# Optimization experiments

Hardware: AMD Instinct MI355X
Metric: run time of the kernel (lower is better)

## Reference

```python
import jax, jax.numpy as jnp
import numpy as np

E = 8
DIMS = [512, 1024, 1024, 512]
BATCH = 2048


def _init_w(key, shape):
    a = np.sqrt(6.0 / (shape[-2] * shape[-1]))
    return jax.random.uniform(key, shape, dtype=jnp.float32, minval=-a, maxval=a)


def setup_inputs() -> dict:
    key = jax.random.key(0)
    ks = jax.random.split(key, 8)
    inp = {
        "weight_blend": jax.random.uniform(ks[0], (BATCH, E), dtype=jnp.float32),
        "x": jax.random.normal(ks[1], (BATCH, DIMS[0]), dtype=jnp.float32),
    }
    for i in range(3):
        inp[f"W{i}"] = _init_w(ks[2 + i], (E, DIMS[i + 1], DIMS[i]))
        inp[f"B{i}"] = jnp.zeros((E, DIMS[i + 1], 1), dtype=jnp.float32)
    return inp


def reference(weight_blend, x, W0, B0, W1, B1, W2, B2):
    Ws = [W0, W1, W2]
    Bs = [B0, B1, B2]
    acts = [jax.nn.elu, jax.nn.elu, None]
    for W, B, act in zip(Ws, Bs, acts):
        # dropout p=0 -> identity
        # blended-expert GEMM: sum_e wb[b,e] * (W[e] @ x[b]) == einsum
        t = jnp.einsum("be,eoi,bi->bo", weight_blend, W, x)
        bias = jnp.einsum("be,eo->bo", weight_blend, B[..., 0])
        x = t + bias
        if act is not None:
            x = act(x)
    return x
```

## Files before the change

### kernel.cpp

```cpp
#include <hip/hip_runtime.h>
#include <math.h>

typedef __attribute__((ext_vector_type(8))) short bf16x8;
typedef __attribute__((ext_vector_type(4))) float f32x4;

#define NEXP 8
#define BATCH 2048

__device__ __forceinline__ unsigned short f2bf(float f) {
    union { float f; unsigned u; } v; v.f = f;
    unsigned r = v.u + 0x7FFFu + ((v.u >> 16) & 1u);
    return (unsigned short)(r >> 16);
}

__global__ __launch_bounds__(256) void pack_all(
    const float* __restrict__ W0, const float* __restrict__ W1,
    const float* __restrict__ W2, const float* __restrict__ x,
    unsigned short* __restrict__ W0p, unsigned short* __restrict__ W1p,
    unsigned short* __restrict__ W2p, unsigned short* __restrict__ x0p)
{
    __shared__ float T[128 * 36];
    const int bid = blockIdx.x, t = threadIdx.x;

    if (bid < 10240) {
        const float* W; unsigned short* out; int KB, Din, Dout, U, lin;
        if (bid < 2048)      { W = W0; out = W0p; KB = 16; Din = 512;  Dout = 1024; U = 4; lin = bid; }
        else if (bid < 6144) { W = W1; out = W1p; KB = 32; Din = 1024; Dout = 1024; U = 4; lin = bid - 2048; }
        else                 { W = W2; out = W2p; KB = 32; Din = 1024; Dout = 512;  U = 2; lin = bid - 6144; }
        const int e  = lin & 7;
        const int r  = lin >> 3;
        const int kb = r % KB;
        const int nb = r / KB;
        const int N0 = nb * 16 * U;
        const int K0 = kb * 32;
        for (int it = 0; it < U / 2; ++it) {
            const int idx = t + 256 * it;
            const int nl = idx >> 3, k4 = (idx & 7) * 4;
            float4 v = *(const float4*)(W + ((size_t)e * Dout + N0 + nl) * Din + K0 + k4);
            *(float4*)(T + nl * 36 + k4) = v;
        }
        __syncthreads();
        if (t < 64 * U) {
            const int u = t >> 6, l = t & 63;
            const float* p = T + (u * 16 + (l & 15)) * 36 + (l >> 4) * 8;
            bf16x8 h;
            #pragma unroll
            for (int j = 0; j < 8; ++j) h[j] = (short)f2bf(p[j]);
            *(bf16x8*)(out + (size_t)lin * (U * 512) + t * 8) = h;
        }
    } else {
        const int lin = bid - 10240;
        const int kb = lin & 15, mb = lin >> 4;
        for (int it = 0; it < 4; ++it) {
            const int idx = t + 256 * it;
            const int ml = idx >> 3, k4 = (idx & 7) * 4;
            float4 v = *(const float4*)(x + (size_t)(mb * 128 + ml) * 512 + kb * 32 + k4);
            *(float4*)(T + ml * 36 + k4) = v;
        }
        __syncthreads();
        #pragma unroll
        for (int it = 0; it < 2; ++it) {
            const int s = t + 256 * it;
            const int g = s >> 6, l = s & 63;
            const float* p = T + (g * 16 + (l & 15)) * 36 + (l >> 4) * 8;
            bf16x8 h;
            #pragma unroll
            for (int j = 0; j < 8; ++j) h[j] = (short)f2bf(p[j]);
            *(bf16x8*)(x0p + (size_t)lin * 4096 + s * 8) = h;
        }
    }
}

template<int UP>
__global__ __launch_bounds__(256, 3) void moe_mfma6(
    const unsigned short* __restrict__ Xp,
    const unsigned short* __restrict__ Wp,
    const float* __restrict__ Bias,
    const float* __restrict__ WBl,
    void* __restrict__ Yout,
    int KB, int Dout, int KBn, int act, int packed_out)
{
    constexpr int PSTR = 36;
    __shared__ __align__(16) float lds_f[2 * 64 * PSTR];

    const int tid  = threadIdx.x;
    const int ew   = tid >> 6;
    const int l    = tid & 63;
    const int lh   = l >> 4;
    const int ll   = l & 15;
    const int e0   = 2 * ew;
    const int bx   = blockIdx.x;
    const int by   = blockIdx.y;
    const int m0   = by * 64;
    const int n0   = bx * 32;
    const int mb   = by >> 1;
    const int half = by & 1;

    f32x4 acc0[4][2], acc1[4][2];
    #pragma unroll
    for (int t = 0; t < 4; ++t)
        #pragma unroll
        for (int u = 0; u < 2; ++u)
            #pragma unroll
            for (int i = 0; i < 4; ++i) { acc0[t][u][i] = 0.f; acc1[t][u][i] = 0.f; }

    unsigned aoff[4];
    #pragma unroll
    for (int t = 0; t < 4; ++t)
        aoff[t] = (unsigned)(mb * KB) * 8192u + (unsigned)(half * 4 + t) * 1024u + l * 16u;
    const int nb   = (bx * 2) / UP;
    const int uoff = (bx * 2) % UP;
    unsigned boff0[2], boff1[2];
    #pragma unroll
    for (int u = 0; u < 2; ++u) {
        boff0[u] = (((unsigned)(nb * KB) * 8 + e0) * UP + uoff + u) * 1024u + l * 16u;
        boff1[u] = boff0[u] + UP * 1024u;
    }
    const unsigned astr = 8192u;
    const unsigned bstr = UP * 8192u;
    const char* xc = (const char*)Xp;
    const char* wc = (const char*)Wp;

    bf16x8 aR[2][4], b0R[2][2], b1R[2][2];

    auto LOAD = [&](int s, int kk) {
        const unsigned ab = (unsigned)kk * astr;
        const unsigned bb = (unsigned)kk * bstr;
        #pragma unroll
        for (int t = 0; t < 4; ++t)
            aR[s][t] = *(const bf16x8*)(xc + aoff[t] + ab);
        #pragma unroll
        for (int u = 0; u < 2; ++u) {
            b0R[s][u] = *(const bf16x8*)(wc + boff0[u] + bb);
            b1R[s][u] = *(const bf16x8*)(wc + boff1[u] + bb);
        }
    };
    auto MF = [&](int s) {
        #pragma unroll
        for (int u = 0; u < 2; ++u)
            #pragma unroll
            for (int t = 0; t < 4; ++t) {
                acc0[t][u] = __builtin_amdgcn_mfma_f32_16x16x32_bf16(aR[s][t], b0R[s][u], acc0[t][u], 0, 0, 0);
                acc1[t][u] = __builtin_amdgcn_mfma_f32_16x16x32_bf16(aR[s][t], b1R[s][u], acc1[t][u], 0, 0, 0);
            }
    };

    LOAD(0, 0);
    for (int kk = 0; kk < KB; kk += 2) {
        if (kk + 1 < KB) LOAD(1, kk + 1);
        MF(0);
        if (kk + 2 < KB) LOAD(0, kk + 2);
        MF(1);
    }

    float bi0[2], bi1[2];
    #pragma unroll
    for (int u = 0; u < 2; ++u) {
        const int n = n0 + u * 16 + ll;
        bi0[u] = Bias[(size_t)e0 * Dout + n];
        bi1[u] = Bias[(size_t)(e0 + 1) * Dout + n];
    }

    float* pb = lds_f + (ew & 1) * (64 * PSTR);

    if (ew < 2) {
        #pragma unroll
        for (int t = 0; t < 4; ++t)
            #pragma unroll
            for (int r = 0; r < 4; ++r) {
                const int lm = 16 * t + 4 * lh + r;
                float2 wbp = ((const float2*)(WBl + (size_t)(m0 + lm) * NEXP))[ew];
                #pragma unroll
                for (int u = 0; u < 2; ++u)
                    pb[lm * PSTR + u * 16 + ll] =
                        wbp.x * (acc0[t][u][r] + bi0[u]) + wbp.y * (acc1[t][u][r] + bi1[u]);
            }
    }
    __syncthreads();
    if (ew >= 2) {
        #pragma unroll
        for (int t = 0; t < 4; ++t)
            #pragma unroll
            for (int r = 0; r < 4; ++r) {
                const int lm = 16 * t + 4 * lh + r;
                float2 wbp = ((const float2*)(WBl + (size_t)(m0 + lm) * NEXP))[ew];
                #pragma unroll
                for (int u = 0; u < 2; ++u)
                    pb[lm * PSTR + u * 16 + ll] +=
                        wbp.x * (acc0[t][u][r] + bi0[u]) + wbp.y * (acc1[t][u][r] + bi1[u]);
            }
    }
    __syncthreads();

    float* pb0 = lds_f;
    float* pb1 = lds_f + 64 * PSTR;
    if (packed_out) {
        const int g  = tid >> 6;
        const int c0 = lh * 8;
        const int rowbase = (g * 16 + ll) * PSTR;
        bf16x8 h;
        #pragma unroll
        for (int j = 0; j < 8; ++j) {
            float v = pb0[rowbase + c0 + j] + pb1[rowbase + c0 + j];
            if (act) v = v > 0.f ? v : expm1f(v);
            h[j] = (short)f2bf(v);
        }
        unsigned short* dst = (unsigned short*)Yout +
            ((size_t)(mb * KBn + bx) * 8 + half * 4 + g) * 512 + l * 8;
        *(bf16x8*)dst = h;
    } else {
        #pragma unroll
        for (int it = 0; it < 2; ++it) {
            const int idx = tid + 256 * it;
            const int row = idx >> 3;
            const int c4  = (idx & 7) * 4;
            float4 s = *(const float4*)(pb0 + row * PSTR + c4);
            float4 q = *(const float4*)(pb1 + row * PSTR + c4);
            s.x += q.x; s.y += q.y; s.z += q.z; s.w += q.w;
            if (act) {
                s.x = s.x > 0.f ? s.x : expm1f(s.x);
                s.y = s.y > 0.f ? s.y : expm1f(s.y);
                s.z = s.z > 0.f ? s.z : expm1f(s.z);
                s.w = s.w > 0.f ? s.w : expm1f(s.w);
            }
            *(float4*)((float*)Yout + (size_t)(m0 + row) * Dout + n0 + c4) = s;
        }
    }
}

#define BM 64
#define BNF 64
#define BKF 16
#define PAD 4

__global__ __launch_bounds__(256) void moe_layer_f32(
    const float* __restrict__ X, const float* __restrict__ W,
    const float* __restrict__ Bias, const float* __restrict__ WB,
    float* __restrict__ Y, int Din, int Dout, int act)
{
    __shared__ float As[BKF][BM + PAD];
    __shared__ float Bs[BKF][BNF + PAD];
    const int tid = threadIdx.x;
    const int tm = tid >> 4, tn = tid & 15;
    const int m0 = blockIdx.y * BM, n0 = blockIdx.x * BNF;
    const int lr = tid >> 2, lc = (tid & 3) << 2;
    float acc[4][4] = {};
    const float* xrow  = X  + (size_t)(m0 + lr) * Din;
    const float* wbrow = WB + (size_t)(m0 + lr) * NEXP;
    const float* wrow0 = W  + (size_t)(n0 + lr) * Din;
    for (int e = 0; e < NEXP; ++e) {
        const float wbe = wbrow[e];
        const float* wrow = wrow0 + (size_t)e * Dout * Din;
        for (int k0 = 0; k0 < Din; k0 += BKF) {
            float4 av = *(const float4*)(xrow + k0 + lc);
            float4 bv = *(const float4*)(wrow + k0 + lc);
            __syncthreads();
            As[lc+0][lr] = av.x*wbe; As[lc+1][lr] = av.y*wbe;
            As[lc+2][lr] = av.z*wbe; As[lc+3][lr] = av.w*wbe;
            Bs[lc+0][lr] = bv.x; Bs[lc+1][lr] = bv.y;
            Bs[lc+2][lr] = bv.z; Bs[lc+3][lr] = bv.w;
            __syncthreads();
            #pragma unroll
            for (int k = 0; k < BKF; ++k) {
                float4 a = *(const float4*)&As[k][tm << 2];
                float4 b = *(const float4*)&Bs[k][tn << 2];
                acc[0][0]+=a.x*b.x; acc[0][1]+=a.x*b.y; acc[0][2]+=a.x*b.z; acc[0][3]+=a.x*b.w;
                acc[1][0]+=a.y*b.x; acc[1][1]+=a.y*b.y; acc[1][2]+=a.y*b.z; acc[1][3]+=a.y*b.w;
                acc[2][0]+=a.z*b.x; acc[2][1]+=a.z*b.y; acc[2][2]+=a.z*b.z; acc[2][3]+=a.z*b.w;
                acc[3][0]+=a.w*b.x; acc[3][1]+=a.w*b.y; acc[3][2]+=a.w*b.z; acc[3][3]+=a.w*b.w;
            }
        }
    }
    #pragma unroll
    for (int im = 0; im < 4; ++im) {
        const int m = m0 + (tm << 2) + im;
        const float* wbm = WB + (size_t)m * NEXP;
        float wv[NEXP];
        #pragma unroll
        for (int e = 0; e < NEXP; ++e) wv[e] = wbm[e];
        #pragma unroll
        for (int in = 0; in < 4; ++in) {
            const int n = n0 + (tn << 2) + in;
            float bsum = 0.f;
            #pragma unroll
            for (int e = 0; e < NEXP; ++e) bsum += wv[e] * Bias[(size_t)e * Dout + n];
            float v = acc[im][in] + bsum;
            if (act) v = v > 0.f ? v : expm1f(v);
            acc[im][in] = v;
        }
        float4 o = make_float4(acc[im][0], acc[im][1], acc[im][2], acc[im][3]);
        *(float4*)(Y + (size_t)m * Dout + n0 + (tn << 2)) = o;
    }
}

extern "C" void kernel_launch(void* const* d_in, const int* in_sizes, int n_in,
                              void* d_out, int out_size, void* d_ws, size_t ws_size,
                              hipStream_t stream)
{
    (void)in_sizes; (void)n_in; (void)out_size;
    const float* wb = (const float*)d_in[0];
    const float* x  = (const float*)d_in[1];
    const float* W0 = (const float*)d_in[2];
    const float* B0 = (const float*)d_in[3];
    const float* W1 = (const float*)d_in[4];
    const float* B1 = (const float*)d_in[5];
    const float* W2 = (const float*)d_in[6];
    const float* B2 = (const float*)d_in[7];
    float* out = (float*)d_out;

    const size_t NW0 = (size_t)8*1024*512, NW1 = (size_t)8*1024*1024, NW2 = (size_t)8*512*1024;
    const size_t NX0 = (size_t)BATCH*512, NX1 = (size_t)BATCH*1024;
    const size_t need = (NW0 + NW1 + NW2 + NX0 + 2 * NX1) * 2;

    if (ws_size >= need) {
        unsigned short* W0p = (unsigned short*)d_ws;
        unsigned short* W1p = W0p + NW0;
        unsigned short* W2p = W1p + NW1;
        unsigned short* x0p = W2p + NW2;
        unsigned short* x1p = x0p + NX0;
        unsigned short* x2p = x1p + NX1;
        pack_all<<<10496, 256, 0, stream>>>(W0, W1, W2, x, W0p, W1p, W2p, x0p);
        moe_mfma6<4><<<dim3(32, 32), 256, 0, stream>>>(x0p, W0p, B0, wb, x1p, 16, 1024, 32, 1, 1);
        moe_mfma6<4><<<dim3(32, 32), 256, 0, stream>>>(x1p, W1p, B1, wb, x2p, 32, 1024, 32, 1, 1);
        moe_mfma6<2><<<dim3(16, 32), 256, 0, stream>>>(x2p, W2p, B2, wb, out, 32, 512,  0, 0, 0);
    } else {
        float* x1 = (float*)d_ws;
        float* x2 = x1 + (size_t)BATCH * 1024;
        moe_layer_f32<<<dim3(1024/BNF, BATCH/BM), 256, 0, stream>>>(x,  W0, B0, wb, x1, 512,  1024, 1);
        moe_layer_f32<<<dim3(1024/BNF, BATCH/BM), 256, 0, stream>>>(x1, W1, B1, wb, x2, 1024, 1024, 1);
        moe_layer_f32<<<dim3(512/BNF,  BATCH/BM), 256, 0, stream>>>(x2, W2, B2, wb, out, 1024, 512,  0);
    }
}
```

Before: 201.8 us.

## Switch MoE GEMMs to 32x32x16 MFMA with new packing and split-K last layer

```diff
diff --git a/kernel.cpp b/kernel.cpp
--- a/kernel.cpp
+++ b/kernel.cpp
@@ -1,8 +1,8 @@
 #include <hip/hip_runtime.h>
 #include <math.h>
 
-typedef __attribute__((ext_vector_type(8))) short bf16x8;
-typedef __attribute__((ext_vector_type(4))) float f32x4;
+typedef __attribute__((ext_vector_type(8)))  short bf16x8;
+typedef __attribute__((ext_vector_type(16))) float f32x16;
 
 #define NEXP 8
 #define BATCH 2048
@@ -13,136 +13,124 @@
     return (unsigned short)(r >> 16);
 }
 
-__global__ __launch_bounds__(256) void pack_all(
+__global__ __launch_bounds__(256) void pack32(
     const float* __restrict__ W0, const float* __restrict__ W1,
     const float* __restrict__ W2, const float* __restrict__ x,
     unsigned short* __restrict__ W0p, unsigned short* __restrict__ W1p,
     unsigned short* __restrict__ W2p, unsigned short* __restrict__ x0p)
 {
-    __shared__ float T[128 * 36];
-    const int bid = blockIdx.x, t = threadIdx.x;
-
-    if (bid < 10240) {
-        const float* W; unsigned short* out; int KB, Din, Dout, U, lin;
-        if (bid < 2048)      { W = W0; out = W0p; KB = 16; Din = 512;  Dout = 1024; U = 4; lin = bid; }
-        else if (bid < 6144) { W = W1; out = W1p; KB = 32; Din = 1024; Dout = 1024; U = 4; lin = bid - 2048; }
-        else                 { W = W2; out = W2p; KB = 32; Din = 1024; Dout = 512;  U = 2; lin = bid - 6144; }
-        const int e  = lin & 7;
-        const int r  = lin >> 3;
-        const int kb = r % KB;
-        const int nb = r / KB;
-        const int N0 = nb * 16 * U;
-        const int K0 = kb * 32;
-        for (int it = 0; it < U / 2; ++it) {
-            const int idx = t + 256 * it;
-            const int nl = idx >> 3, k4 = (idx & 7) * 4;
-            float4 v = *(const float4*)(W + ((size_t)e * Dout + N0 + nl) * Din + K0 + k4);
-            *(float4*)(T + nl * 36 + k4) = v;
-        }
-        __syncthreads();
-        if (t < 64 * U) {
-            const int u = t >> 6, l = t & 63;
-            const float* p = T + (u * 16 + (l & 15)) * 36 + (l >> 4) * 8;
-            bf16x8 h;
-            #pragma unroll
-            for (int j = 0; j < 8; ++j) h[j] = (short)f2bf(p[j]);
-            *(bf16x8*)(out + (size_t)lin * (U * 512) + t * 8) = h;
-        }
+    __shared__ float T[32 * 260];
+    const int bid = blockIdx.x, tid = threadIdx.x;
+
+    const float* src; unsigned short* out;
+    int Din, rowbase, kc, KBw, lin_nb_e_base; bool isx = false;
+    if (bid < 512) {
+        int c = bid;            const int e = c & 7, kcl = (c >> 3) & 1, nb = c >> 4;
+        src = W0; out = W0p; Din = 512; KBw = 32; kc = kcl;
+        rowbase = e * 1024 + nb * 32; lin_nb_e_base = (nb * KBw) * 8 + e;
+    } else if (bid < 1536) {
+        int c = bid - 512;      const int e = c & 7, kcl = (c >> 3) & 3, nb = c >> 5;
+        src = W1; out = W1p; Din = 1024; KBw = 64; kc = kcl;
+        rowbase = e * 1024 + nb * 32; lin_nb_e_base = (nb * KBw) * 8 + e;
+    } else if (bid < 2048) {
+        int c = bid - 1536;     const int e = c & 7, kcl = (c >> 3) & 3, nb = c >> 5;
+        src = W2; out = W2p; Din = 1024; KBw = 64; kc = kcl;
+        rowbase = e * 512 + nb * 32; lin_nb_e_base = (nb * KBw) * 8 + e;
     } else {
-        const int lin = bid - 10240;
-        const int kb = lin & 15, mb = lin >> 4;
-        for (int it = 0; it < 4; ++it) {
-            const int idx = t + 256 * it;
-            const int ml = idx >> 3, k4 = (idx & 7) * 4;
-            float4 v = *(const float4*)(x + (size_t)(mb * 128 + ml) * 512 + kb * 32 + k4);
-            *(float4*)(T + ml * 36 + k4) = v;
-        }
-        __syncthreads();
-        #pragma unroll
-        for (int it = 0; it < 2; ++it) {
-            const int s = t + 256 * it;
-            const int g = s >> 6, l = s & 63;
-            const float* p = T + (g * 16 + (l & 15)) * 36 + (l >> 4) * 8;
-            bf16x8 h;
-            #pragma unroll
-            for (int j = 0; j < 8; ++j) h[j] = (short)f2bf(p[j]);
-            *(bf16x8*)(x0p + (size_t)lin * 4096 + s * 8) = h;
-        }
-    }
-}
-
-template<int UP>
-__global__ __launch_bounds__(256, 3) void moe_mfma6(
+        int c = bid - 2048;     const int kcl = c & 1, mb = c >> 1;
+        src = x; out = x0p; Din = 512; KBw = 32; kc = kcl;
+        rowbase = mb * 32; lin_nb_e_base = mb * 32; isx = true;
+    }
+
+    #pragma unroll
+    for (int it = 0; it < 8; ++it) {
+        const int idx = tid + 256 * it;
+        const int row = idx >> 6, c4 = idx & 63;
+        float4 v = *(const float4*)(src + (size_t)(rowbase + row) * Din + kc * 256 + c4 * 4);
+        *(float4*)(T + row * 260 + c4 * 4) = v;
+    }
+    __syncthreads();
+    #pragma unroll
+    for (int it = 0; it < 4; ++it) {
+        const int s = tid + 256 * it;
+        const int f = s >> 6, l = s & 63;
+        const float* p = T + (l & 31) * 260 + f * 16 + (l >> 5) * 8;
+        bf16x8 h;
+        #pragma unroll
+        for (int j = 0; j < 8; ++j) h[j] = (short)f2bf(p[j]);
+        const int lin = isx ? (lin_nb_e_base + kc * 16 + f)
+                            : (lin_nb_e_base + (kc * 16 + f) * 8);
+        *(bf16x8*)(out + (size_t)lin * 512 + l * 8) = h;
+    }
+}
+
+__global__ __launch_bounds__(256, 2) void moe_gemm32(
     const unsigned short* __restrict__ Xp,
     const unsigned short* __restrict__ Wp,
     const float* __restrict__ Bias,
     const float* __restrict__ WBl,
     void* __restrict__ Yout,
-    int KB, int Dout, int KBn, int act, int packed_out)
-{
-    constexpr int PSTR = 36;
-    __shared__ __align__(16) float lds_f[2 * 64 * PSTR];
-
-    const int tid  = threadIdx.x;
-    const int ew   = tid >> 6;
-    const int l    = tid & 63;
-    const int lh   = l >> 4;
-    const int ll   = l & 15;
-    const int e0   = 2 * ew;
-    const int bx   = blockIdx.x;
-    const int by   = blockIdx.y;
-    const int m0   = by * 64;
-    const int n0   = bx * 32;
-    const int mb   = by >> 1;
-    const int half = by & 1;
-
-    f32x4 acc0[4][2], acc1[4][2];
-    #pragma unroll
-    for (int t = 0; t < 4; ++t)
-        #pragma unroll
-        for (int u = 0; u < 2; ++u)
-            #pragma unroll
-            for (int i = 0; i < 4; ++i) { acc0[t][u][i] = 0.f; acc1[t][u][i] = 0.f; }
-
-    unsigned aoff[4];
-    #pragma unroll
-    for (int t = 0; t < 4; ++t)
-        aoff[t] = (unsigned)(mb * KB) * 8192u + (unsigned)(half * 4 + t) * 1024u + l * 16u;
-    const int nb   = (bx * 2) / UP;
-    const int uoff = (bx * 2) % UP;
-    unsigned boff0[2], boff1[2];
-    #pragma unroll
-    for (int u = 0; u < 2; ++u) {
-        boff0[u] = (((unsigned)(nb * KB) * 8 + e0) * UP + uoff + u) * 1024u + l * 16u;
-        boff1[u] = boff0[u] + UP * 1024u;
-    }
-    const unsigned astr = 8192u;
-    const unsigned bstr = UP * 8192u;
+    int KB, int kk0, int Dout, int KBx, int KBn, int act,
+    int addbias, int packed_out)
+{
+    __shared__ __align__(16) float lds_f[2 * 64 * 68];
+
+    const int tid = threadIdx.x;
+    const int ew  = tid >> 6;
+    const int l   = tid & 63;
+    const int ln  = l & 31;
+    const int lk  = l >> 5;
+    const int e0  = 2 * ew;
+    const int bx  = blockIdx.x;
+    const int by  = blockIdx.y;
+    const int m0  = by * 64;
+    const int n0  = bx * 64;
+
+    f32x16 acc[2][2][2];
+    #pragma unroll
+    for (int e = 0; e < 2; ++e)
+        #pragma unroll
+        for (int t = 0; t < 2; ++t)
+            #pragma unroll
+            for (int u = 0; u < 2; ++u)
+                #pragma unroll
+                for (int i = 0; i < 16; ++i) acc[e][t][u][i] = 0.f;
+
+    unsigned aoff[2], boff[2][2];
+    #pragma unroll
+    for (int t = 0; t < 2; ++t)
+        aoff[t] = ((unsigned)(by * 2 + t) * KBx + kk0) * 1024u + l * 16u;
+    #pragma unroll
+    for (int u = 0; u < 2; ++u)
+        #pragma unroll
+        for (int e = 0; e < 2; ++e)
+            boff[e][u] = (((unsigned)(bx * 2 + u) * KBx + kk0) * 8 + e0 + e) * 1024u + l * 16u;
     const char* xc = (const char*)Xp;
     const char* wc = (const char*)Wp;
 
-    bf16x8 aR[2][4], b0R[2][2], b1R[2][2];
+    bf16x8 aR[2][2], bR[2][2][2];
 
     auto LOAD = [&](int s, int kk) {
-        const unsigned ab = (unsigned)kk * astr;
-        const unsigned bb = (unsigned)kk * bstr;
-        #pragma unroll
-        for (int t = 0; t < 4; ++t)
+        const unsigned ab = (unsigned)kk * 1024u;
+        const unsigned bb = (unsigned)kk * 8192u;
+        #pragma unroll
+        for (int t = 0; t < 2; ++t)
             aR[s][t] = *(const bf16x8*)(xc + aoff[t] + ab);
         #pragma unroll
-        for (int u = 0; u < 2; ++u) {
-            b0R[s][u] = *(const bf16x8*)(wc + boff0[u] + bb);
-            b1R[s][u] = *(const bf16x8*)(wc + boff1[u] + bb);
-        }
+        for (int e = 0; e < 2; ++e)
+            #pragma unroll
+            for (int u = 0; u < 2; ++u)
+                bR[s][e][u] = *(const bf16x8*)(wc + boff[e][u] + bb);
     };
     auto MF = [&](int s) {
         #pragma unroll
-        for (int u = 0; u < 2; ++u)
-            #pragma unroll
-            for (int t = 0; t < 4; ++t) {
-                acc0[t][u] = __builtin_amdgcn_mfma_f32_16x16x32_bf16(aR[s][t], b0R[s][u], acc0[t][u], 0, 0, 0);
-                acc1[t][u] = __builtin_amdgcn_mfma_f32_16x16x32_bf16(aR[s][t], b1R[s][u], acc1[t][u], 0, 0, 0);
-            }
+        for (int e = 0; e < 2; ++e)
+            #pragma unroll
+            for (int u = 0; u < 2; ++u)
+                #pragma unroll
+                for (int t = 0; t < 2; ++t)
+                    acc[e][t][u] = __builtin_amdgcn_mfma_f32_32x32x16_bf16(
+                        aR[s][t], bR[s][e][u], acc[e][t][u], 0, 0, 0);
     };
 
     LOAD(0, 0);
@@ -153,79 +141,92 @@
         MF(1);
     }
 
-    float bi0[2], bi1[2];
-    #pragma unroll
-    for (int u = 0; u < 2; ++u) {
-        const int n = n0 + u * 16 + ll;
-        bi0[u] = Bias[(size_t)e0 * Dout + n];
-        bi1[u] = Bias[(size_t)(e0 + 1) * Dout + n];
-    }
-
-    float* pb = lds_f + (ew & 1) * (64 * PSTR);
+    float bi[2][2];
+    #pragma unroll
+    for (int e = 0; e < 2; ++e)
+        #pragma unroll
+        for (int u = 0; u < 2; ++u)
+            bi[e][u] = addbias ? Bias[(size_t)(e0 + e) * Dout + n0 + u * 32 + ln] : 0.f;
+
+    float* pb = lds_f + (ew & 1) * (64 * 68);
 
     if (ew < 2) {
         #pragma unroll
-        for (int t = 0; t < 4; ++t)
-            #pragma unroll
-            for (int r = 0; r < 4; ++r) {
-                const int lm = 16 * t + 4 * lh + r;
-                float2 wbp = ((const float2*)(WBl + (size_t)(m0 + lm) * NEXP))[ew];
+        for (int t = 0; t < 2; ++t)
+            #pragma unroll
+            for (int r = 0; r < 16; ++r) {
+                const int row = t * 32 + (r & 3) + 8 * (r >> 2) + 4 * lk;
+                float2 wbp = ((const float2*)(WBl + (size_t)(m0 + row) * NEXP))[ew];
                 #pragma unroll
                 for (int u = 0; u < 2; ++u)
-                    pb[lm * PSTR + u * 16 + ll] =
-                        wbp.x * (acc0[t][u][r] + bi0[u]) + wbp.y * (acc1[t][u][r] + bi1[u]);
+                    pb[row * 68 + u * 32 + ln] =
+                        wbp.x * (acc[0][t][u][r] + bi[0][u]) + wbp.y * (acc[1][t][u][r] + bi[1][u]);
             }
     }
     __syncthreads();
     if (ew >= 2) {
         #pragma unroll
-        for (int t = 0; t < 4; ++t)
-            #pragma unroll
-            for (int r = 0; r < 4; ++r) {
-                const int lm = 16 * t + 4 * lh + r;
-                float2 wbp = ((const float2*)(WBl + (size_t)(m0 + lm) * NEXP))[ew];
+        for (int t = 0; t < 2; ++t)
+            #pragma unroll
+            for (int r = 0; r < 16; ++r) {
+                const int row = t * 32 + (r & 3) + 8 * (r >> 2) + 4 * lk;
+                float2 wbp = ((const float2*)(WBl + (size_t)(m0 + row) * NEXP))[ew];
                 #pragma unroll
                 for (int u = 0; u < 2; ++u)
-                    pb[lm * PSTR + u * 16 + ll] +=
-                        wbp.x * (acc0[t][u][r] + bi0[u]) + wbp.y * (acc1[t][u][r] + bi1[u]);
+                    pb[row * 68 + u * 32 + ln] +=
+                        wbp.x * (acc[0][t][u][r] + bi[0][u]) + wbp.y * (acc[1][t][u][r] + bi[1][u]);
             }
     }
     __syncthreads();
 
     float* pb0 = lds_f;
-    float* pb1 = lds_f + 64 * PSTR;
+    float* pb1 = lds_f + 64 * 68;
     if (packed_out) {
-        const int g  = tid >> 6;
-        const int c0 = lh * 8;
-        const int rowbase = (g * 16 + ll) * PSTR;
-        bf16x8 h;
-        #pragma unroll
-        for (int j = 0; j < 8; ++j) {
-            float v = pb0[rowbase + c0 + j] + pb1[rowbase + c0 + j];
-            if (act) v = v > 0.f ? v : expm1f(v);
-            h[j] = (short)f2bf(v);
-        }
-        unsigned short* dst = (unsigned short*)Yout +
-            ((size_t)(mb * KBn + bx) * 8 + half * 4 + g) * 512 + l * 8;
-        *(bf16x8*)dst = h;
+        #pragma unroll
+        for (int it = 0; it < 2; ++it) {
+            const int s = tid + 256 * it;
+            const int f = s >> 6, l2 = s & 63;
+            const int row = (f & 1) * 32 + (l2 & 31);
+            const int cb  = (f >> 1) * 16 + (l2 >> 5) * 8;
+            bf16x8 h;
+            #pragma unroll
+            for (int j = 0; j < 8; ++j) {
+                float v = pb0[row * 68 + cb + j] + pb1[row * 68 + cb + j];
+                if (act) v = v > 0.f ? v : expm1f(v);
+                h[j] = (short)f2bf(v);
+            }
+            const unsigned lin = (unsigned)(by * 2 + (f & 1)) * KBn + bx * 4 + (f >> 1);
+            *(bf16x8*)((unsigned short*)Yout + (size_t)lin * 512 + l2 * 8) = h;
+        }
     } else {
         #pragma unroll
-        for (int it = 0; it < 2; ++it) {
-            const int idx = tid + 256 * it;
-            const int row = idx >> 3;
-            const int c4  = (idx & 7) * 4;
-            float4 s = *(const float4*)(pb0 + row * PSTR + c4);
-            float4 q = *(const float4*)(pb1 + row * PSTR + c4);
-            s.x += q.x; s.y += q.y; s.z += q.z; s.w += q.w;
+        for (int it = 0; it < 4; ++it) {
+            const int s = tid + 256 * it;
+            const int row = s >> 4, c4 = (s & 15) * 4;
+            float4 a = *(const float4*)(pb0 + row * 68 + c4);
+            float4 b = *(const float4*)(pb1 + row * 68 + c4);
+            a.x += b.x; a.y += b.y; a.z += b.z; a.w += b.w;
             if (act) {
-                s.x = s.x > 0.f ? s.x : expm1f(s.x);
-                s.y = s.y > 0.f ? s.y : expm1f(s.y);
-                s.z = s.z > 0.f ? s.z : expm1f(s.z);
-                s.w = s.w > 0.f ? s.w : expm1f(s.w);
-            }
-            *(float4*)((float*)Yout + (size_t)(m0 + row) * Dout + n0 + c4) = s;
-        }
-    }
+                a.x = a.x > 0.f ? a.x : expm1f(a.x);
+                a.y = a.y > 0.f ? a.y : expm1f(a.y);
+                a.z = a.z > 0.f ? a.z : expm1f(a.z);
+                a.w = a.w > 0.f ? a.w : expm1f(a.w);
+            }
+            *(float4*)((float*)Yout + (size_t)(m0 + row) * Dout + n0 + c4) = a;
+        }
+    }
+}
+
+__global__ __launch_bounds__(256) void reduce2(
+    const float* __restrict__ p0, const float* __restrict__ p1,
+    float* __restrict__ out, int n4)
+{
+    int i = blockIdx.x * blockDim.x + threadIdx.x;
+    if (i >= n4) return;
+    float4 a = ((const float4*)p0)[i];
+    float4 b = ((const float4*)p1)[i];
+    a.x += b.x; a.y += b.y; a.z += b.z; a.w += b.w;
+    ((float4*)out)[i] = a;
 }
 
 #define BM 64
@@ -310,19 +311,33 @@
 
     const size_t NW0 = (size_t)8*1024*512, NW1 = (size_t)8*1024*1024, NW2 = (size_t)8*512*1024;
     const size_t NX0 = (size_t)BATCH*512, NX1 = (size_t)BATCH*1024;
-    const size_t need = (NW0 + NW1 + NW2 + NX0 + 2 * NX1) * 2;
-
-    if (ws_size >= need) {
+    const size_t need_main  = (NW0 + NW1 + NW2 + NX0 + 2 * NX1) * 2;
+    const size_t need_split = need_main + 2 * (size_t)BATCH * 512 * 4;
+
+    if (ws_size >= need_main) {
         unsigned short* W0p = (unsigned short*)d_ws;
         unsigned short* W1p = W0p + NW0;
         unsigned short* W2p = W1p + NW1;
         unsigned short* x0p = W2p + NW2;
         unsigned short* x1p = x0p + NX0;
         unsigned short* x2p = x1p + NX1;
-        pack_all<<<10496, 256, 0, stream>>>(W0, W1, W2, x, W0p, W1p, W2p, x0p);
-        moe_mfma6<4><<<dim3(32, 32), 256, 0, stream>>>(x0p, W0p, B0, wb, x1p, 16, 1024, 32, 1, 1);
-        moe_mfma6<4><<<dim3(32, 32), 256, 0, stream>>>(x1p, W1p, B1, wb, x2p, 32, 1024, 32, 1, 1);
-        moe_mfma6<2><<<dim3(16, 32), 256, 0, stream>>>(x2p, W2p, B2, wb, out, 32, 512,  0, 0, 0);
+        pack32<<<2176, 256, 0, stream>>>(W0, W1, W2, x, W0p, W1p, W2p, x0p);
+        moe_gemm32<<<dim3(16, 32), 256, 0, stream>>>(x0p, W0p, B0, wb, x1p,
+                                                     32, 0, 1024, 32, 64, 1, 1, 1);
+        moe_gemm32<<<dim3(16, 32), 256, 0, stream>>>(x1p, W1p, B1, wb, x2p,
+                                                     64, 0, 1024, 64, 64, 1, 1, 1);
+        if (ws_size >= need_split) {
+            float* p0 = (float*)(x2p + NX1);
+            float* p1 = p0 + (size_t)BATCH * 512;
+            moe_gemm32<<<dim3(8, 32), 256, 0, stream>>>(x2p, W2p, B2, wb, p0,
+                                                        32, 0, 512, 64, 0, 0, 1, 0);
+            moe_gemm32<<<dim3(8, 32), 256, 0, stream>>>(x2p, W2p, B2, wb, p1,
+                                                        32, 32, 512, 64, 0, 0, 0, 0);
+            reduce2<<<1024, 256, 0, stream>>>(p0, p1, out, BATCH * 512 / 4);
+        } else {
+            moe_gemm32<<<dim3(8, 32), 256, 0, stream>>>(x2p, W2p, B2, wb, out,
+                                                        64, 0, 512, 64, 0, 0, 1, 0);
+        }
     } else {
         float* x1 = (float*)d_ws;
         float* x2 = x1 + (size_t)BATCH * 1024;
```

Result: slower. 217.7 us (+7.9%).
